# Kernel tuning notes

Hardware: AMD Instinct MI355X
Metric: run time of the kernel (lower is better)

Reference implementation:

```python
import jax, jax.numpy as jnp
import numpy as np

B, R, S, T, D, DK = 256, 196, 200, 50, 512, 100


def setup_inputs() -> dict:
    key = jax.random.key(0)
    ks = jax.random.split(key, 20)
    inp = {
        'ifeature': jax.random.normal(ks[0], (B, R, D), jnp.float32),
        'tfeature_h': jax.random.normal(ks[1], (B, S, D), jnp.float32),
        'gfeature': jax.random.normal(ks[2], (B, S, D), jnp.float32),
        'efeature': jax.random.normal(ks[3], (B, T, D), jnp.float32),
    }
    # learned params (keras 'random_normal' init ~ stddev 0.05, 'zeros' for biases)
    lens = [R, S, S, T]
    for i in range(4):
        inp[f'w_vi{i}'] = 0.05 * jax.random.normal(ks[4 + 4 * i], (D, DK), jnp.float32)
        inp[f'w_vt{i}'] = 0.05 * jax.random.normal(ks[5 + 4 * i], (D, DK), jnp.float32)
        inp[f'w_p{i}'] = 0.05 * jax.random.normal(ks[6 + 4 * i], (2 * DK, 1), jnp.float32)
        inp[f'b{i}'] = jnp.zeros((lens[i],), jnp.float32)
    return inp


def _attend(feats, w_feat, vec, w_vec, w_p, b, vec_first):
    # feats: [B,N,D], vec: [B,D]. Score = concat(tanh parts) @ w_p + b.
    # concat+dense == split w_p into the two halves and add the partial scores.
    k = w_feat.shape[1]
    sf = jnp.tanh(jnp.einsum('bnd,dk->bnk', feats, w_feat))  # [B,N,k]
    sv = jnp.tanh(vec @ w_vec)                               # [B,k]
    if vec_first:
        wv, wf = w_p[:k, 0], w_p[k:, 0]
    else:
        wf, wv = w_p[:k, 0], w_p[k:, 0]
    score = sf @ wf + (sv @ wv)[:, None] + b                 # [B,N]
    p = jax.nn.softmax(score, axis=-1)
    return jnp.einsum('bn,bnd->bd', p, feats)                # [B,D]


def reference(ifeature, tfeature_h, gfeature, efeature,
              w_vi0, w_vt0, w_p0, b0,
              w_vi1, w_vt1, w_p1, b1,
              w_vi2, w_vt2, w_p2, b2,
              w_vi3, w_vt3, w_p3, b3):
    tfeature = jnp.mean(tfeature_h, axis=1)                  # [B,D]
    # block 0: attend over image regions, concat order (image, text)
    Vi = _attend(ifeature, w_vi0, tfeature, w_vt0, w_p0, b0, vec_first=False)
    # block 1: attend over text tokens, concat order (Vi, text)
    Vt = _attend(tfeature_h, w_vt1, Vi, w_vi1, w_p1, b1, vec_first=True)
    # block 2: attend over group feature with query Vi+Vt
    Vg = _attend(gfeature, w_vt2, Vi + Vt, w_vi2, w_p2, b2, vec_first=True)
    # block 3: attend over title feature with query Vi+Vt
    Ve = _attend(efeature, w_vt3, Vi + Vt, w_vi3, w_p3, b3, vec_first=True)
    return Vi + Vt + 0.5 * Vg + 0.5 * Ve
```

## Files before the change

### kernel.cpp

```cpp
#include <hip/hip_runtime.h>

#define DD 512
#define DKk 100
#define NT 7
#define CHUNK 16
#define MAXN 208
#define LDS_STRIDE 520

typedef __attribute__((ext_vector_type(8))) short short8;
typedef __attribute__((ext_vector_type(4))) short short4v;
typedef __attribute__((ext_vector_type(4))) float f32x4;

struct AttendArgs {
  const float* feats[4];
  const float* wfeat[4];
  const float* wf[4];
  const float* bias[4];
  int   N[4];
  float coef[4];
};

__device__ __forceinline__ short f2bf(float x) {
  unsigned u = __builtin_bit_cast(unsigned, x);
  unsigned r = (u + 0x7fffu + ((u >> 16) & 1u)) >> 16;
  return (short)r;
}

__device__ __forceinline__ float fast_tanh(float x) {
  const float e = __expf(2.0f * x);
  return 1.0f - 2.0f / (e + 1.0f);
}

__global__ void wprep_kernel(AttendArgs args, unsigned short* __restrict__ wfrag) {
  const int a = blockIdx.x / NT;
  const int t = blockIdx.x % NT;
  const int tid = threadIdx.x;
  const int lane = tid & 63;
  const int m = lane & 15;
  const int q = lane >> 4;
  const int kg = tid >> 6;
  const int col = t * 16 + m;
  const float* __restrict__ w = args.wfeat[a];
  unsigned short* __restrict__ dst = wfrag + (size_t)((a * NT + t) * 16) * 512;
  #pragma unroll
  for (int i = 0; i < 4; ++i) {
    const int ks = kg * 4 + i;
    short8 v;
    #pragma unroll
    for (int j = 0; j < 8; ++j) {
      const int d = ks * 32 + q * 8 + j;
      v[j] = (col < DKk) ? f2bf(w[d * DKk + col]) : (short)0;
    }
    *reinterpret_cast<short8*>(dst + (size_t)ks * 512 + lane * 8) = v;
  }
}

__global__ __launch_bounds__(512, 2)
void fused_kernel(AttendArgs args, const unsigned short* __restrict__ wfrag,
                  float* __restrict__ out) {
  const int a = blockIdx.x & 3;
  const int b = blockIdx.x >> 2;
  const int tid = threadIdx.x;
  const int lane = tid & 63;
  const int wave = tid >> 6;
  const int m = lane & 15;
  const int q = lane >> 4;
  const int N = args.N[a];
  const float* __restrict__ feats = args.feats[a] + (size_t)b * (size_t)N * DD;
  const float* __restrict__ wfp = args.wf[a];
  const float* __restrict__ bias = args.bias[a];

  __shared__ __align__(16) unsigned short f_lds[2][CHUNK][LDS_STRIDE];
  __shared__ float sc_part[8][MAXN];
  __shared__ float red[512];
  __shared__ float p_lds[MAXN];

  short8 bfrag[16];
  float wfv = 0.f;
  if (wave < NT) {
    const int col = wave * 16 + m;
    wfv = (col < DKk) ? wfp[col] : 0.f;
    const unsigned short* src = wfrag + (size_t)((a * NT + wave) * 16) * 512 + lane * 8;
    #pragma unroll
    for (int ks = 0; ks < 16; ++ks)
      bfrag[ks] = *reinterpret_cast<const short8*>(src + (size_t)ks * 512);
  } else {
    #pragma unroll
    for (int ks = 0; ks < 16; ++ks) bfrag[ks] = short8(0);
  }

  const int nchunks = (N + CHUNK - 1) / CHUNK;

  float4 pf[4];
  #pragma unroll
  for (int it = 0; it < 4; ++it) {
    const int idx = tid + it * 512;
    const int row = idx >> 7;
    const int c4 = idx & 127;
    pf[it] = (row < N)
      ? *reinterpret_cast<const float4*>(feats + (size_t)row * DD + (c4 << 2))
      : make_float4(0.f, 0.f, 0.f, 0.f);
  }

  for (int c = 0; c < nchunks; ++c) {
    const int bufc = c & 1;
    #pragma unroll
    for (int it = 0; it < 4; ++it) {
      const int idx = tid + it * 512;
      const int row = idx >> 7;
      const int c4 = idx & 127;
      short4v pk = { f2bf(pf[it].x), f2bf(pf[it].y), f2bf(pf[it].z), f2bf(pf[it].w) };
      *reinterpret_cast<short4v*>(&f_lds[bufc][row][c4 << 2]) = pk;
    }
    if (c + 1 < nchunks) {
      const int n0n = (c + 1) * CHUNK;
      #pragma unroll
      for (int it = 0; it < 4; ++it) {
        const int idx = tid + it * 512;
        const int row = n0n + (idx >> 7);
        const int c4 = idx & 127;
        pf[it] = (row < N)
          ? *reinterpret_cast<const float4*>(feats + (size_t)row * DD + (c4 << 2))
          : make_float4(0.f, 0.f, 0.f, 0.f);
      }
    }
    __syncthreads();

    if (wave < NT) {
      f32x4 acc = {0.f, 0.f, 0.f, 0.f};
      #pragma unroll
      for (int ks = 0; ks < 16; ++ks) {
        const short8 af = *reinterpret_cast<const short8*>(&f_lds[bufc][m][ks * 32 + q * 8]);
        acc = __builtin_amdgcn_mfma_f32_16x16x32_bf16(af, bfrag[ks], acc, 0, 0, 0);
      }
      float part[4];
      #pragma unroll
      for (int r = 0; r < 4; ++r) part[r] = fast_tanh(acc[r]) * wfv;
      #pragma unroll
      for (int mask = 1; mask <= 8; mask <<= 1) {
        #pragma unroll
        for (int r = 0; r < 4; ++r) part[r] += __shfl_xor(part[r], mask, 64);
      }
      if (m == 0) {
        #pragma unroll
        for (int r = 0; r < 4; ++r) sc_part[wave][c * 16 + q * 4 + r] = part[r];
      }
    } else if (m == 0) {
      #pragma unroll
      for (int r = 0; r < 4; ++r) sc_part[7][c * 16 + q * 4 + r] = 0.f;
    }
  }
  __syncthreads();

  float sval = -1e30f;
  if (tid < N) {
    sval = sc_part[0][tid] + sc_part[1][tid] + sc_part[2][tid] + sc_part[3][tid]
         + sc_part[4][tid] + sc_part[5][tid] + sc_part[6][tid] + sc_part[7][tid]
         + bias[tid];
  }
  red[tid] = sval;
  __syncthreads();
  for (int s = 256; s > 0; s >>= 1) {
    if (tid < s) red[tid] = fmaxf(red[tid], red[tid + s]);
    __syncthreads();
  }
  const float mx = red[0];
  __syncthreads();
  const float e = (tid < N) ? __expf(sval - mx) : 0.f;
  if (tid < MAXN) p_lds[tid] = e;
  red[tid] = e;
  __syncthreads();
  for (int s = 256; s > 0; s >>= 1) {
    if (tid < s) red[tid] += red[tid + s];
    __syncthreads();
  }
  const float scale = args.coef[a] / red[0];

  float acc0 = 0.f, acc1 = 0.f;
  const float* __restrict__ fp = feats + tid;
  const int n4 = N & ~3;
  for (int n = 0; n < n4; n += 4) {
    acc0 += p_lds[n + 0] * fp[(size_t)(n + 0) * DD];
    acc1 += p_lds[n + 1] * fp[(size_t)(n + 1) * DD];
    acc0 += p_lds[n + 2] * fp[(size_t)(n + 2) * DD];
    acc1 += p_lds[n + 3] * fp[(size_t)(n + 3) * DD];
  }
  for (int n = n4; n < N; ++n)
    acc0 += p_lds[n] * fp[(size_t)n * DD];
  atomicAdd(&out[(size_t)b * DD + tid], (acc0 + acc1) * scale);
}

extern "C" void kernel_launch(void* const* d_in, const int* in_sizes, int n_in,
                              void* d_out, int out_size, void* d_ws, size_t ws_size,
                              hipStream_t stream) {
  AttendArgs args;
  args.feats[0] = (const float*)d_in[0];
  args.wfeat[0] = (const float*)d_in[4];
  args.wf[0]    = (const float*)d_in[6];
  args.bias[0]  = (const float*)d_in[7];
  args.N[0] = 196; args.coef[0] = 1.0f;

  args.feats[1] = (const float*)d_in[1];
  args.wfeat[1] = (const float*)d_in[9];
  args.wf[1]    = (const float*)d_in[10] + 100;
  args.bias[1]  = (const float*)d_in[11];
  args.N[1] = 200; args.coef[1] = 1.0f;

  args.feats[2] = (const float*)d_in[2];
  args.wfeat[2] = (const float*)d_in[13];
  args.wf[2]    = (const float*)d_in[14] + 100;
  args.bias[2]  = (const float*)d_in[15];
  args.N[2] = 200; args.coef[2] = 0.5f;

  args.feats[3] = (const float*)d_in[3];
  args.wfeat[3] = (const float*)d_in[17];
  args.wf[3]    = (const float*)d_in[18] + 100;
  args.bias[3]  = (const float*)d_in[19];
  args.N[3] = 50;  args.coef[3] = 0.5f;

  unsigned short* wfrag = (unsigned short*)d_ws;

  hipMemsetAsync(d_out, 0, (size_t)out_size * sizeof(float), stream);
  wprep_kernel<<<dim3(4 * NT), dim3(256), 0, stream>>>(args, wfrag);
  fused_kernel<<<dim3(4 * 256), dim3(512), 0, stream>>>(args, wfrag, (float*)d_out);
}
```

Measured before the change: 396.5 us.

## Fuse online softmax and weighted sum into chunk loop using LDS bf16 features

Replaces the post-loop score reduction, block-wide max/sum trees and the second global pass over feats with a flash-attention style online softmax. Each chunk's scores are accumulated through LDS atomics, and every thread updates its running max, normalizer and output from the bf16 features already staged in LDS. This removes the second global read of the features and many barriers, and launch bounds are raised for more occupancy. In exchange the weighted sum now uses bf16-rounded features, which lowers accuracy, and it adds LDS atomics and an extra barrier per chunk.

```diff
diff --git a/kernel.cpp b/kernel.cpp
--- a/kernel.cpp
+++ b/kernel.cpp
@@ -4,7 +4,6 @@
 #define DKk 100
 #define NT 7
 #define CHUNK 16
-#define MAXN 208
 #define LDS_STRIDE 520
 
 typedef __attribute__((ext_vector_type(8))) short short8;
@@ -24,6 +23,11 @@
   unsigned u = __builtin_bit_cast(unsigned, x);
   unsigned r = (u + 0x7fffu + ((u >> 16) & 1u)) >> 16;
   return (short)r;
+}
+
+__device__ __forceinline__ float bf2f(unsigned short b) {
+  unsigned u = ((unsigned)b) << 16;
+  return __builtin_bit_cast(float, u);
 }
 
 __device__ __forceinline__ float fast_tanh(float x) {
@@ -55,7 +59,7 @@
   }
 }
 
-__global__ __launch_bounds__(512, 2)
+__global__ __launch_bounds__(512, 4)
 void fused_kernel(AttendArgs args, const unsigned short* __restrict__ wfrag,
                   float* __restrict__ out) {
   const int a = blockIdx.x & 3;
@@ -71,9 +75,7 @@
   const float* __restrict__ bias = args.bias[a];
 
   __shared__ __align__(16) unsigned short f_lds[2][CHUNK][LDS_STRIDE];
-  __shared__ float sc_part[8][MAXN];
-  __shared__ float red[512];
-  __shared__ float p_lds[MAXN];
+  __shared__ float score_lds[2][CHUNK];
 
   short8 bfrag[16];
   float wfv = 0.f;
@@ -84,12 +86,11 @@
     #pragma unroll
     for (int ks = 0; ks < 16; ++ks)
       bfrag[ks] = *reinterpret_cast<const short8*>(src + (size_t)ks * 512);
-  } else {
-    #pragma unroll
-    for (int ks = 0; ks < 16; ++ks) bfrag[ks] = short8(0);
   }
 
   const int nchunks = (N + CHUNK - 1) / CHUNK;
+
+  float O = 0.f, m_run = -1e30f, l_run = 0.f;
 
   float4 pf[4];
   #pragma unroll
@@ -104,6 +105,7 @@
 
   for (int c = 0; c < nchunks; ++c) {
     const int bufc = c & 1;
+    const int n0 = c * CHUNK;
     #pragma unroll
     for (int it = 0; it < 4; ++it) {
       const int idx = tid + it * 512;
@@ -112,8 +114,12 @@
       short4v pk = { f2bf(pf[it].x), f2bf(pf[it].y), f2bf(pf[it].z), f2bf(pf[it].w) };
       *reinterpret_cast<short4v*>(&f_lds[bufc][row][c4 << 2]) = pk;
     }
+    if (tid < CHUNK)
+      score_lds[bufc][tid] = (n0 + tid < N) ? bias[n0 + tid] : -1e30f;
+    __syncthreads();
+
     if (c + 1 < nchunks) {
-      const int n0n = (c + 1) * CHUNK;
+      const int n0n = n0 + CHUNK;
       #pragma unroll
       for (int it = 0; it < 4; ++it) {
         const int idx = tid + it * 512;
@@ -124,7 +130,6 @@
           : make_float4(0.f, 0.f, 0.f, 0.f);
       }
     }
-    __syncthreads();
 
     if (wave < NT) {
       f32x4 acc = {0.f, 0.f, 0.f, 0.f};
@@ -143,51 +148,33 @@
       }
       if (m == 0) {
         #pragma unroll
-        for (int r = 0; r < 4; ++r) sc_part[wave][c * 16 + q * 4 + r] = part[r];
-      }
-    } else if (m == 0) {
-      #pragma unroll
-      for (int r = 0; r < 4; ++r) sc_part[7][c * 16 + q * 4 + r] = 0.f;
-    }
-  }
-  __syncthreads();
-
-  float sval = -1e30f;
-  if (tid < N) {
-    sval = sc_part[0][tid] + sc_part[1][tid] + sc_part[2][tid] + sc_part[3][tid]
-         + sc_part[4][tid] + sc_part[5][tid] + sc_part[6][tid] + sc_part[7][tid]
-         + bias[tid];
-  }
-  red[tid] = sval;
-  __syncthreads();
-  for (int s = 256; s > 0; s >>= 1) {
-    if (tid < s) red[tid] = fmaxf(red[tid], red[tid + s]);
+        for (int r = 0; r < 4; ++r)
+          atomicAdd(&score_lds[bufc][q * 4 + r], part[r]);
+      }
+    }
     __syncthreads();
-  }
-  const float mx = red[0];
-  __syncthreads();
-  const float e = (tid < N) ? __expf(sval - mx) : 0.f;
-  if (tid < MAXN) p_lds[tid] = e;
-  red[tid] = e;
-  __syncthreads();
-  for (int s = 256; s > 0; s >>= 1) {
-    if (tid < s) red[tid] += red[tid + s];
-    __syncthreads();
-  }
-  const float scale = args.coef[a] / red[0];
-
-  float acc0 = 0.f, acc1 = 0.f;
-  const float* __restrict__ fp = feats + tid;
-  const int n4 = N & ~3;
-  for (int n = 0; n < n4; n += 4) {
-    acc0 += p_lds[n + 0] * fp[(size_t)(n + 0) * DD];
-    acc1 += p_lds[n + 1] * fp[(size_t)(n + 1) * DD];
-    acc0 += p_lds[n + 2] * fp[(size_t)(n + 2) * DD];
-    acc1 += p_lds[n + 3] * fp[(size_t)(n + 3) * DD];
-  }
-  for (int n = n4; n < N; ++n)
-    acc0 += p_lds[n] * fp[(size_t)n * DD];
-  atomicAdd(&out[(size_t)b * DD + tid], (acc0 + acc1) * scale);
+
+    float m_new = m_run;
+    #pragma unroll
+    for (int i = 0; i < CHUNK; ++i) m_new = fmaxf(m_new, score_lds[bufc][i]);
+    const float alpha = __expf(m_run - m_new);
+    float o = O * alpha;
+    float esum0 = 0.f, esum1 = 0.f;
+    float o1 = 0.f;
+    #pragma unroll
+    for (int i = 0; i < CHUNK; i += 2) {
+      const float e0 = __expf(score_lds[bufc][i] - m_new);
+      const float e1 = __expf(score_lds[bufc][i + 1] - m_new);
+      esum0 += e0; esum1 += e1;
+      o  += e0 * bf2f(f_lds[bufc][i][tid]);
+      o1 += e1 * bf2f(f_lds[bufc][i + 1][tid]);
+    }
+    O = o + o1;
+    l_run = l_run * alpha + esum0 + esum1;
+    m_run = m_new;
+  }
+
+  atomicAdd(&out[(size_t)b * DD + tid], args.coef[a] * O / l_run);
 }
 
 extern "C" void kernel_launch(void* const* d_in, const int* in_sizes, int n_in,
```

Result: slower. 410.6 us (+3.5%).
